# Performance work log

Hardware: AMD Instinct MI355X
Metric: run time of the kernel (lower is better)

The kernel has to match this reference:

```python
import jax, jax.numpy as jnp
import numpy as np

B, S, D_IN, D_OUT, R = 8, 2048, 2048, 2048, 16

def setup_inputs() -> dict:
    key = jax.random.key(0)
    k = jax.random.split(key, 5)
    scale_w = 1.0 / np.sqrt(D_IN)
    return {
        "x": jax.random.normal(k[0], (B, S, D_IN), dtype=jnp.float32),
        "A_params": jax.random.normal(k[1], (B, D_OUT, R), dtype=jnp.float32) * 0.02,
        "B_params": jax.random.normal(k[2], (B, R, D_IN), dtype=jnp.float32) * 0.02,
        "W": jax.random.normal(k[3], (D_OUT, D_IN), dtype=jnp.float32) * scale_w,
        "b": jax.random.normal(k[4], (D_OUT,), dtype=jnp.float32) * scale_w,
    }

def reference(x, A_params, B_params, W, b):
    # base: x @ W^T + b  -> [B, S, out]
    base_out = jnp.einsum("bsi,oi->bso", x, W) + b
    # intermediate = x @ B^T -> [B, S, r]
    intermediate = jnp.einsum("bsi,bri->bsr", x, B_params)
    # adaptation = intermediate @ A^T -> [B, S, out]
    adaptation = jnp.einsum("bsr,bor->bso", intermediate, A_params)
    return base_out + adaptation
```

## Files before the change

kernel.cpp:

```cpp
#include <hip/hip_runtime.h>
#include <cstdint>
#include <cstddef>

typedef __attribute__((ext_vector_type(4))) float  floatx4;
typedef __attribute__((ext_vector_type(8))) __bf16 bf16x8;
typedef __attribute__((ext_vector_type(8))) unsigned short u16x8;

#define M_TOT 16384
#define N_TOT 2048
#define K_TOT 2048
#define NBATCH 8
#define RLORA 16
#define NT 32

__device__ __forceinline__ unsigned short f32_to_bf16(float f) {
  unsigned u = __float_as_uint(f);
  u += 0x7fffu + ((u >> 16) & 1u);
  return (unsigned short)(u >> 16);
}

__device__ __forceinline__ u16x8 cvt8(const float4& a, const float4& b) {
  u16x8 o;
  o[0] = f32_to_bf16(a.x); o[1] = f32_to_bf16(a.y);
  o[2] = f32_to_bf16(a.z); o[3] = f32_to_bf16(a.w);
  o[4] = f32_to_bf16(b.x); o[5] = f32_to_bf16(b.y);
  o[6] = f32_to_bf16(b.z); o[7] = f32_to_bf16(b.w);
  return o;
}

#define GLOAD_LDS16(gp, lp)                                                        \
  __builtin_amdgcn_global_load_lds((__attribute__((address_space(1))) void*)(void*)(gp), \
                                   (__attribute__((address_space(3))) void*)(void*)(lp), \
                                   16, 0, 0)

template<int V> struct IC { static constexpr int value = V; };

__global__ void k_convert_x(const float* __restrict__ in, unsigned short* __restrict__ out) {
  int i0 = blockIdx.x * blockDim.x + threadIdx.x;
  #pragma unroll
  for (int it = 0; it < 8; ++it) {
    size_t i = (size_t)i0 + (size_t)it * 524288;
    const float4* p = (const float4*)in + i * 2;
    *(u16x8*)(out + i * 8) = cvt8(p[0], p[1]);
  }
}

__global__ void k_convert_small(const float* __restrict__ W, const float* __restrict__ Bp,
                                const float* __restrict__ Ap,
                                unsigned short* __restrict__ wbf, unsigned short* __restrict__ bpbf,
                                unsigned short* __restrict__ abf) {
  int b = blockIdx.x;
  if (b < 2048) {
    int i = b * 256 + threadIdx.x;
    const float4* p = (const float4*)W + (size_t)i * 2;
    *(u16x8*)(wbf + (size_t)i * 8) = cvt8(p[0], p[1]);
  } else if (b < 2176) {
    int i = (b - 2048) * 256 + threadIdx.x;
    const float4* p = (const float4*)Bp + (size_t)i * 2;
    *(u16x8*)(bpbf + (size_t)i * 8) = cvt8(p[0], p[1]);
  } else {
    int row = (b - 2176) * 256 + threadIdx.x;
    const float4* p = (const float4*)(Ap + (size_t)row * RLORA);
    u16x8 lo = cvt8(p[0], p[1]), hi2 = cvt8(p[2], p[3]), z = {0,0,0,0,0,0,0,0};
    u16x8* dst = (u16x8*)(abf + (size_t)row * 32);
    dst[0] = lo; dst[1] = hi2; dst[2] = z; dst[3] = z;
  }
}

__global__ __launch_bounds__(256) void k_inter(const unsigned short* __restrict__ xbf,
                                               const unsigned short* __restrict__ bpbf,
                                               unsigned short* __restrict__ interbf) {
  const int tid  = threadIdx.x;
  const int lane = tid & 63;
  const int wv   = tid >> 6;
  const int l15  = lane & 15;
  const int hi   = lane >> 4;
  const int m0   = blockIdx.x * 64;
  const int bb   = m0 >> 11;

  floatx4 zero = {0.f, 0.f, 0.f, 0.f};
  floatx4 acc[4] = {zero, zero, zero, zero};

  const unsigned short* bpb = bpbf + (size_t)bb * (RLORA * K_TOT);
  const int kb0 = wv * 512;
  for (int kb = kb0; kb < kb0 + 512; kb += 32) {
    bf16x8 bfr = *(const bf16x8*)(bpb + (size_t)l15 * K_TOT + kb + hi * 8);
    #pragma unroll
    for (int mi = 0; mi < 4; ++mi) {
      bf16x8 afr = *(const bf16x8*)(xbf + (size_t)(m0 + mi * 16 + l15) * K_TOT + kb + hi * 8);
      acc[mi] = __builtin_amdgcn_mfma_f32_16x16x32_bf16(afr, bfr, acc[mi], 0, 0, 0);
    }
  }

  __shared__ floatx4 red[4][4][64];
  #pragma unroll
  for (int mi = 0; mi < 4; ++mi) red[wv][mi][lane] = acc[mi];
  __syncthreads();
  if (wv == 0) {
    #pragma unroll
    for (int mi = 0; mi < 4; ++mi) {
      floatx4 s = red[0][mi][lane] + red[1][mi][lane] + red[2][mi][lane] + red[3][mi][lane];
      #pragma unroll
      for (int j = 0; j < 4; ++j) {
        int m = m0 + mi * 16 + hi * 4 + j;
        interbf[(size_t)m * 32 + l15] = f32_to_bf16(s[j]);
        interbf[(size_t)m * 32 + 16 + l15] = 0;
      }
    }
  }
}

#define STAGE_A(bufi, h, tt) do {                                                      \
  GLOAD_LDS16(Ag + (h)*262144 + (tt)*64 + gOff0, AsB + ((bufi)*2+(h))*16384 + ldsB0);  \
  GLOAD_LDS16(Ag + (h)*262144 + (tt)*64 + gOff1, AsB + ((bufi)*2+(h))*16384 + ldsB1);  \
} while(0)
#define STAGE_B(bufi, h, tt) do {                                                      \
  GLOAD_LDS16(Bg + (h)*262144 + (tt)*64 + gOff0, BsB + ((bufi)*2+(h))*16384 + ldsB0);  \
  GLOAD_LDS16(Bg + (h)*262144 + (tt)*64 + gOff1, BsB + ((bufi)*2+(h))*16384 + ldsB1);  \
} while(0)
#define RDA_(B2, q, mi, ks) (*(const bf16x8*)(AsB + (B2)*32768 + aBase + (q)*4096 + (mi)*2048 + koff[ks]))
#define RDB_(B2, ni, ks)    (*(const bf16x8*)(BsB + (B2)*32768 + bBase + (ni)*2048 + koff[ks]))
#define BAR() __builtin_amdgcn_s_barrier()

__global__ __launch_bounds__(512, 2) void k_gemm(const unsigned short* __restrict__ xbf,
                                                 const unsigned short* __restrict__ wbf,
                                                 const unsigned short* __restrict__ interbf,
                                                 const unsigned short* __restrict__ abf,
                                                 const float* __restrict__ bias,
                                                 float* __restrict__ out) {
  __shared__ unsigned short As[2][2][8192];
  __shared__ unsigned short Bs[2][2][8192];
  const int tid  = threadIdx.x;
  const int lane = tid & 63;
  const int wid  = tid >> 6;
  const int wm   = wid >> 2;
  const int wn   = wid & 3;
  const int l15  = lane & 15;
  const int hi   = lane >> 4;
  const int swz  = l15 & 7;

  int bid  = blockIdx.x;
  int swzb = ((bid & 7) << 6) | (bid >> 3);
  const int mt = swzb >> 3;
  const int nt = swzb & 7;
  const int mrow0 = mt << 8;
  const int ncol0 = nt << 8;
  const int bb = mrow0 >> 11;

  const int m0 = mrow0 + wm * 128;
  const int n0 = ncol0 + wn * 64;

  const unsigned short* Ag = xbf + (size_t)mrow0 * K_TOT;
  const unsigned short* Bg = wbf + (size_t)ncol0 * K_TOT;
  char* AsB = (char*)As;
  char* BsB = (char*)Bs;

  const int r0    = tid >> 3;
  const int k80   = (tid & 7) ^ (r0 & 7);
  const int gOff0 = r0 * K_TOT + k80 * 8;
  const int gOff1 = gOff0 + 64 * K_TOT;
  const int ldsB0 = wid * 1024;
  const int ldsB1 = 8192 + wid * 1024;

  const int aBase = wm * 16384 + l15 * 128;
  const int bBase = (wn >> 1) * 16384 + (wn & 1) * 8192 + l15 * 128;
  int koff[2];
  koff[0] = ((0 * 4 + hi) ^ swz) * 16;
  koff[1] = ((1 * 4 + hi) ^ swz) * 16;

  floatx4 acc[8][4];
  bf16x8 bfr[4][2];
  bf16x8 af[2][2];

  {
    bf16x8 la[8], lb[4];
    #pragma unroll
    for (int mi = 0; mi < 8; ++mi)
      la[mi] = *(const bf16x8*)(interbf + (size_t)(m0 + mi * 16 + l15) * 32 + hi * 8);
    #pragma unroll
    for (int ni = 0; ni < 4; ++ni)
      lb[ni] = *(const bf16x8*)(abf + ((size_t)bb * N_TOT + n0 + ni * 16 + l15) * 32 + hi * 8);

    STAGE_A(0, 0, 0); STAGE_A(0, 1, 0); STAGE_B(0, 0, 0); STAGE_B(0, 1, 0);
    STAGE_B(1, 0, 1); STAGE_B(1, 1, 1);

    floatx4 z = {0.f, 0.f, 0.f, 0.f};
    #pragma unroll
    for (int mi = 0; mi < 8; ++mi)
      #pragma unroll
      for (int ni = 0; ni < 4; ++ni)
        acc[mi][ni] = __builtin_amdgcn_mfma_f32_16x16x32_bf16(la[mi], lb[ni], z, 0, 0, 0);
  }
  asm volatile("s_waitcnt vmcnt(4)" ::: "memory");
  BAR();

  auto tile_step = [&](int t, auto bufc, auto sac, auto sbc, auto vmc) {
    constexpr int BUF = decltype(bufc)::value;
    constexpr int SA  = decltype(sac)::value;
    constexpr int SB  = decltype(sbc)::value;
    constexpr int VM  = decltype(vmc)::value;

    #pragma unroll
    for (int ni = 0; ni < 4; ++ni) { bfr[ni][0] = RDB_(BUF, ni, 0); bfr[ni][1] = RDB_(BUF, ni, 1); }
    #pragma unroll
    for (int mi = 0; mi < 2; ++mi) { af[mi][0] = RDA_(BUF, 0, mi, 0); af[mi][1] = RDA_(BUF, 0, mi, 1); }
    if constexpr (SA) STAGE_A(BUF ^ 1, 0, t + 1);
    BAR();
    asm volatile("s_waitcnt lgkmcnt(0)" ::: "memory");
    __builtin_amdgcn_s_setprio(1);
    #pragma unroll
    for (int mi = 0; mi < 2; ++mi)
      #pragma unroll
      for (int ni = 0; ni < 4; ++ni) {
        acc[mi][ni] = __builtin_amdgcn_mfma_f32_16x16x32_bf16(af[mi][0], bfr[ni][0], acc[mi][ni], 0, 0, 0);
        acc[mi][ni] = __builtin_amdgcn_mfma_f32_16x16x32_bf16(af[mi][1], bfr[ni][1], acc[mi][ni], 0, 0, 0);
      }
    __builtin_amdgcn_s_setprio(0);
    BAR();

    #pragma unroll
    for (int mi = 0; mi < 2; ++mi) { af[mi][0] = RDA_(BUF, 1, mi, 0); af[mi][1] = RDA_(BUF, 1, mi, 1); }
    if constexpr (SA) STAGE_A(BUF ^ 1, 1, t + 1);
    BAR();
    asm volatile("s_waitcnt lgkmcnt(0)" ::: "memory");
    __builtin_amdgcn_s_setprio(1);
    #pragma unroll
    for (int mi = 0; mi < 2; ++mi)
      #pragma unroll
      for (int ni = 0; ni < 4; ++ni) {
        acc[2+mi][ni] = __builtin_amdgcn_mfma_f32_16x16x32_bf16(af[mi][0], bfr[ni][0], acc[2+mi][ni], 0, 0, 0);
        acc[2+mi][ni] = __builtin_amdgcn_mfma_f32_16x16x32_bf16(af[mi][1], bfr[ni][1], acc[2+mi][ni], 0, 0, 0);
      }
    __builtin_amdgcn_s_setprio(0);
    BAR();

    #pragma unroll
    for (int mi = 0; mi < 2; ++mi) { af[mi][0] = RDA_(BUF, 2, mi, 0); af[mi][1] = RDA_(BUF, 2, mi, 1); }
    if constexpr (SB) STAGE_B(BUF, 0, t + 2);
    BAR();
    asm volatile("s_waitcnt lgkmcnt(0)" ::: "memory");
    __builtin_amdgcn_s_setprio(1);
    #pragma unroll
    for (int mi = 0; mi < 2; ++mi)
      #pragma unroll
      for (int ni = 0; ni < 4; ++ni) {
        acc[4+mi][ni] = __builtin_amdgcn_mfma_f32_16x16x32_bf16(af[mi][0], bfr[ni][0], acc[4+mi][ni], 0, 0, 0);
        acc[4+mi][ni] = __builtin_amdgcn_mfma_f32_16x16x32_bf16(af[mi][1], bfr[ni][1], acc[4+mi][ni], 0, 0, 0);
      }
    __builtin_amdgcn_s_setprio(0);
    BAR();

    #pragma unroll
    for (int mi = 0; mi < 2; ++mi) { af[mi][0] = RDA_(BUF, 3, mi, 0); af[mi][1] = RDA_(BUF, 3, mi, 1); }
    if constexpr (SB) STAGE_B(BUF, 1, t + 2);
    BAR();
    asm volatile("s_waitcnt lgkmcnt(0)" ::: "memory");
    __builtin_amdgcn_s_setprio(1);
    #pragma unroll
    for (int mi = 0; mi < 2; ++mi)
      #pragma unroll
      for (int ni = 0; ni < 4; ++ni) {
        acc[6+mi][ni] = __builtin_amdgcn_mfma_f32_16x16x32_bf16(af[mi][0], bfr[ni][0], acc[6+mi][ni], 0, 0, 0);
        acc[6+mi][ni] = __builtin_amdgcn_mfma_f32_16x16x32_bf16(af[mi][1], bfr[ni][1], acc[6+mi][ni], 0, 0, 0);
      }
    __builtin_amdgcn_s_setprio(0);
    if constexpr (VM == 4)      asm volatile("s_waitcnt vmcnt(4)" ::: "memory");
    else if constexpr (VM == 0) asm volatile("s_waitcnt vmcnt(0)" ::: "memory");
    BAR();
  };

  for (int t = 0; t < NT - 2; t += 2) {
    tile_step(t,     IC<0>{}, IC<1>{}, IC<1>{}, IC<4>{});
    tile_step(t + 1, IC<1>{}, IC<1>{}, IC<1>{}, IC<4>{});
  }
  tile_step(NT - 2, IC<0>{}, IC<1>{}, IC<0>{}, IC<0>{});
  tile_step(NT - 1, IC<1>{}, IC<0>{}, IC<0>{}, IC<-1>{});

  #pragma unroll
  for (int ni = 0; ni < 4; ++ni) {
    int col = n0 + ni * 16 + l15;
    float bv = bias[col];
    #pragma unroll
    for (int mi = 0; mi < 8; ++mi) {
      int r = m0 + mi * 16 + hi * 4;
      #pragma unroll
      for (int j = 0; j < 4; ++j)
        out[(size_t)(r + j) * N_TOT + col] = acc[mi][ni][j] + bv;
    }
  }
}

extern "C" void kernel_launch(void* const* d_in, const int* in_sizes, int n_in,
                              void* d_out, int out_size, void* d_ws, size_t ws_size,
                              hipStream_t stream) {
  const float* x    = (const float*)d_in[0];
  const float* Ap   = (const float*)d_in[1];
  const float* Bp   = (const float*)d_in[2];
  const float* W    = (const float*)d_in[3];
  const float* bias = (const float*)d_in[4];
  float* out = (float*)d_out;

  char* ws = (char*)d_ws;
  unsigned short* xbf     = (unsigned short*)(ws);
  unsigned short* wbf     = (unsigned short*)(ws + 67108864);
  unsigned short* abf     = (unsigned short*)(ws + 67108864 + 8388608);
  unsigned short* bpbf    = (unsigned short*)(ws + 67108864 + 8388608 + 1048576);
  unsigned short* interbf = (unsigned short*)(ws + 67108864 + 8388608 + 1048576 + 524288);

  k_convert_small<<<dim3(2240), dim3(256), 0, stream>>>(W, Bp, Ap, wbf, bpbf, abf);
  k_convert_x<<<dim3(2048), dim3(256), 0, stream>>>(x, xbf);
  k_inter<<<dim3(256), dim3(256), 0, stream>>>(xbf, bpbf, interbf);
  k_gemm<<<dim3(512), dim3(512), 0, stream>>>(xbf, wbf, interbf, abf, bias, out);
}
```

Measured before the change: 197.6 us.

## Fuse x bf16 conversion with LoRA intermediate projection and drop LDS waits

Merges the x fp32→bf16 conversion kernel with the x·Bᵀ LoRA intermediate kernel. Each block now converts 16 rows of x on the fly, writes the bf16 copy for the main GEMM and feeds the MFMA directly, so the bf16 x is no longer re-read and the separate Bp conversion is gone. It also removes the explicit lgkmcnt(0) waits after barriers in the GEMM main loop and leaves LDS read ordering to the compiler. Each block re-reads and converts its batch's Bp slice in fp32, adding redundant traffic. The GEMM change depends on the compiler inserting the correct waits.

```diff
diff --git a/kernel.cpp b/kernel.cpp
--- a/kernel.cpp
+++ b/kernel.cpp
@@ -35,31 +35,15 @@
 
 template<int V> struct IC { static constexpr int value = V; };
 
-__global__ void k_convert_x(const float* __restrict__ in, unsigned short* __restrict__ out) {
-  int i0 = blockIdx.x * blockDim.x + threadIdx.x;
-  #pragma unroll
-  for (int it = 0; it < 8; ++it) {
-    size_t i = (size_t)i0 + (size_t)it * 524288;
-    const float4* p = (const float4*)in + i * 2;
-    *(u16x8*)(out + i * 8) = cvt8(p[0], p[1]);
-  }
-}
-
-__global__ void k_convert_small(const float* __restrict__ W, const float* __restrict__ Bp,
-                                const float* __restrict__ Ap,
-                                unsigned short* __restrict__ wbf, unsigned short* __restrict__ bpbf,
-                                unsigned short* __restrict__ abf) {
+__global__ void k_convert_small(const float* __restrict__ W, const float* __restrict__ Ap,
+                                unsigned short* __restrict__ wbf, unsigned short* __restrict__ abf) {
   int b = blockIdx.x;
   if (b < 2048) {
     int i = b * 256 + threadIdx.x;
     const float4* p = (const float4*)W + (size_t)i * 2;
     *(u16x8*)(wbf + (size_t)i * 8) = cvt8(p[0], p[1]);
-  } else if (b < 2176) {
-    int i = (b - 2048) * 256 + threadIdx.x;
-    const float4* p = (const float4*)Bp + (size_t)i * 2;
-    *(u16x8*)(bpbf + (size_t)i * 8) = cvt8(p[0], p[1]);
   } else {
-    int row = (b - 2176) * 256 + threadIdx.x;
+    int row = (b - 2048) * 256 + threadIdx.x;
     const float4* p = (const float4*)(Ap + (size_t)row * RLORA);
     u16x8 lo = cvt8(p[0], p[1]), hi2 = cvt8(p[2], p[3]), z = {0,0,0,0,0,0,0,0};
     u16x8* dst = (u16x8*)(abf + (size_t)row * 32);
@@ -67,45 +51,42 @@
   }
 }
 
-__global__ __launch_bounds__(256) void k_inter(const unsigned short* __restrict__ xbf,
-                                               const unsigned short* __restrict__ bpbf,
-                                               unsigned short* __restrict__ interbf) {
+__global__ __launch_bounds__(256) void k_xinter(const float* __restrict__ x,
+                                                const float* __restrict__ Bp,
+                                                unsigned short* __restrict__ xbf,
+                                                unsigned short* __restrict__ interbf) {
   const int tid  = threadIdx.x;
   const int lane = tid & 63;
   const int wv   = tid >> 6;
   const int l15  = lane & 15;
   const int hi   = lane >> 4;
-  const int m0   = blockIdx.x * 64;
+  const int m0   = blockIdx.x * 16;
   const int bb   = m0 >> 11;
 
-  floatx4 zero = {0.f, 0.f, 0.f, 0.f};
-  floatx4 acc[4] = {zero, zero, zero, zero};
-
-  const unsigned short* bpb = bpbf + (size_t)bb * (RLORA * K_TOT);
+  floatx4 acc = {0.f, 0.f, 0.f, 0.f};
+  const float* bpb = Bp + (size_t)bb * (RLORA * K_TOT);
+  const size_t xrow = (size_t)(m0 + l15) * K_TOT;
+  const size_t brow = (size_t)l15 * K_TOT;
   const int kb0 = wv * 512;
   for (int kb = kb0; kb < kb0 + 512; kb += 32) {
-    bf16x8 bfr = *(const bf16x8*)(bpb + (size_t)l15 * K_TOT + kb + hi * 8);
-    #pragma unroll
-    for (int mi = 0; mi < 4; ++mi) {
-      bf16x8 afr = *(const bf16x8*)(xbf + (size_t)(m0 + mi * 16 + l15) * K_TOT + kb + hi * 8);
-      acc[mi] = __builtin_amdgcn_mfma_f32_16x16x32_bf16(afr, bfr, acc[mi], 0, 0, 0);
-    }
-  }
-
-  __shared__ floatx4 red[4][4][64];
-  #pragma unroll
-  for (int mi = 0; mi < 4; ++mi) red[wv][mi][lane] = acc[mi];
+    const float* xp = x + xrow + kb + hi * 8;
+    u16x8 ao = cvt8(*(const float4*)xp, *(const float4*)(xp + 4));
+    *(u16x8*)(xbf + xrow + kb + hi * 8) = ao;
+    const float* bpp = bpb + brow + kb + hi * 8;
+    u16x8 bo = cvt8(*(const float4*)bpp, *(const float4*)(bpp + 4));
+    acc = __builtin_amdgcn_mfma_f32_16x16x32_bf16(*(bf16x8*)&ao, *(bf16x8*)&bo, acc, 0, 0, 0);
+  }
+
+  __shared__ floatx4 red[4][64];
+  red[wv][lane] = acc;
   __syncthreads();
   if (wv == 0) {
-    #pragma unroll
-    for (int mi = 0; mi < 4; ++mi) {
-      floatx4 s = red[0][mi][lane] + red[1][mi][lane] + red[2][mi][lane] + red[3][mi][lane];
-      #pragma unroll
-      for (int j = 0; j < 4; ++j) {
-        int m = m0 + mi * 16 + hi * 4 + j;
-        interbf[(size_t)m * 32 + l15] = f32_to_bf16(s[j]);
-        interbf[(size_t)m * 32 + 16 + l15] = 0;
-      }
+    floatx4 s = red[0][lane] + red[1][lane] + red[2][lane] + red[3][lane];
+    #pragma unroll
+    for (int j = 0; j < 4; ++j) {
+      int m = m0 + hi * 4 + j;
+      interbf[(size_t)m * 32 + l15] = f32_to_bf16(s[j]);
+      interbf[(size_t)m * 32 + 16 + l15] = 0;
     }
   }
 }
@@ -206,7 +187,6 @@
     for (int mi = 0; mi < 2; ++mi) { af[mi][0] = RDA_(BUF, 0, mi, 0); af[mi][1] = RDA_(BUF, 0, mi, 1); }
     if constexpr (SA) STAGE_A(BUF ^ 1, 0, t + 1);
     BAR();
-    asm volatile("s_waitcnt lgkmcnt(0)" ::: "memory");
     __builtin_amdgcn_s_setprio(1);
     #pragma unroll
     for (int mi = 0; mi < 2; ++mi)
@@ -222,7 +202,6 @@
     for (int mi = 0; mi < 2; ++mi) { af[mi][0] = RDA_(BUF, 1, mi, 0); af[mi][1] = RDA_(BUF, 1, mi, 1); }
     if constexpr (SA) STAGE_A(BUF ^ 1, 1, t + 1);
     BAR();
-    asm volatile("s_waitcnt lgkmcnt(0)" ::: "memory");
     __builtin_amdgcn_s_setprio(1);
     #pragma unroll
     for (int mi = 0; mi < 2; ++mi)
@@ -238,7 +217,6 @@
     for (int mi = 0; mi < 2; ++mi) { af[mi][0] = RDA_(BUF, 2, mi, 0); af[mi][1] = RDA_(BUF, 2, mi, 1); }
     if constexpr (SB) STAGE_B(BUF, 0, t + 2);
     BAR();
-    asm volatile("s_waitcnt lgkmcnt(0)" ::: "memory");
     __builtin_amdgcn_s_setprio(1);
     #pragma unroll
     for (int mi = 0; mi < 2; ++mi)
@@ -254,7 +232,6 @@
     for (int mi = 0; mi < 2; ++mi) { af[mi][0] = RDA_(BUF, 3, mi, 0); af[mi][1] = RDA_(BUF, 3, mi, 1); }
     if constexpr (SB) STAGE_B(BUF, 1, t + 2);
     BAR();
-    asm volatile("s_waitcnt lgkmcnt(0)" ::: "memory");
     __builtin_amdgcn_s_setprio(1);
     #pragma unroll
     for (int mi = 0; mi < 2; ++mi)
@@ -304,11 +281,9 @@
   unsigned short* xbf     = (unsigned short*)(ws);
   unsigned short* wbf     = (unsigned short*)(ws + 67108864);
   unsigned short* abf     = (unsigned short*)(ws + 67108864 + 8388608);
-  unsigned short* bpbf    = (unsigned short*)(ws + 67108864 + 8388608 + 1048576);
-  unsigned short* interbf = (unsigned short*)(ws + 67108864 + 8388608 + 1048576 + 524288);
-
-  k_convert_small<<<dim3(2240), dim3(256), 0, stream>>>(W, Bp, Ap, wbf, bpbf, abf);
-  k_convert_x<<<dim3(2048), dim3(256), 0, stream>>>(x, xbf);
-  k_inter<<<dim3(256), dim3(256), 0, stream>>>(xbf, bpbf, interbf);
+  unsigned short* interbf = (unsigned short*)(ws + 67108864 + 8388608 + 1048576);
+
+  k_convert_small<<<dim3(2112), dim3(256), 0, stream>>>(W, Ap, wbf, abf);
+  k_xinter<<<dim3(1024), dim3(256), 0, stream>>>(x, Bp, xbf, interbf);
   k_gemm<<<dim3(512), dim3(512), 0, stream>>>(xbf, wbf, interbf, abf, bias, out);
 }
```

Measured after the change: 192.6 us (median of 2 runs). 1.03x faster.
